# Kernel tuning notes

Hardware: AMD Instinct MI355X
Metric: run time of the kernel (lower is better)

Reference implementation:

```python
import jax, jax.numpy as jnp
import numpy as np

HIDDEN = 128
HEADS = 8
HEAD_DIM = HIDDEN // HEADS
N = 2048
SCALE = HEAD_DIM ** -0.5


def setup_inputs() -> dict:
    key = jax.random.key(0)
    ks = jax.random.split(key, 12)
    # xavier_uniform bound for square (HIDDEN, HIDDEN) weights
    bound = float(np.sqrt(6.0 / (HIDDEN + HIDDEN)))
    def w(k):
        return jax.random.uniform(k, (HIDDEN, HIDDEN), jnp.float32, -bound, bound)
    return {
        "x": jax.random.normal(ks[0], (N, HIDDEN), jnp.float32),
        "attention_bias": jax.random.normal(ks[1], (N, N, HEADS), jnp.float32),
        "key_padding_mask": jnp.zeros((N,), jnp.bool_),
        "Wq": w(ks[2]), "bq": jnp.zeros((HIDDEN,), jnp.float32),
        "Wk": w(ks[3]), "bk": jnp.zeros((HIDDEN,), jnp.float32),
        "Wv": w(ks[4]), "bv": jnp.zeros((HIDDEN,), jnp.float32),
        "Wo": w(ks[5]), "bo": jnp.zeros((HIDDEN,), jnp.float32),
    }


def reference(x, attention_bias, key_padding_mask, Wq, bq, Wk, bk, Wv, bv, Wo, bo):
    n = x.shape[0]
    # torch Linear: y = x @ W.T + b
    q = (x @ Wq.T + bq).reshape(n, HEADS, HEAD_DIM).transpose(1, 0, 2)  # (H, N, D)
    k = (x @ Wk.T + bk).reshape(n, HEADS, HEAD_DIM).transpose(1, 0, 2)
    v = (x @ Wv.T + bv).reshape(n, HEADS, HEAD_DIM).transpose(1, 0, 2)
    scores = jnp.einsum('hnd,hmd->hnm', q, k) * SCALE        # (H, N, N)
    scores = scores + attention_bias.transpose(2, 0, 1)       # additive graph bias
    mask = key_padding_mask[None, None, :]                    # (1, 1, N) over keys
    scores = jnp.where(mask, -jnp.inf, scores)
    attn = jax.nn.softmax(scores, axis=-1)
    out = jnp.einsum('hnm,hmd->hnd', attn, v)                 # (H, N, D)
    out = out.transpose(1, 0, 2).reshape(n, HIDDEN)
    return out @ Wo.T + bo
```

## Files before the change

kernel.cpp:

```cpp
#include <hip/hip_runtime.h>
#include <hip/hip_bf16.h>

#define NSEQ 2048
#define HID 128
#define HEADS 8
#define HD 16
#define SCALE 0.25f
#define TQ 8
#define TK 64
#define SPLIT 4
#define KT_PER (NSEQ / TK / SPLIT)
#define QROW 160
#define SROW 68

typedef unsigned short ushort_t;

__device__ __forceinline__ void unpack2(unsigned u, float& a, float& b) {
    union { unsigned x; float f; } lo, hi;
    lo.x = u << 16; hi.x = u & 0xffff0000u;
    a = lo.f; b = hi.f;
}
__device__ __forceinline__ void unpack8(uint4 u, float* f) {
    unpack2(u.x, f[0], f[1]); unpack2(u.y, f[2], f[3]);
    unpack2(u.z, f[4], f[5]); unpack2(u.w, f[6], f[7]);
}

__global__ void transpose_kernel(const float* __restrict__ Wq, const float* __restrict__ Wk,
                                 const float* __restrict__ Wv, const float* __restrict__ Wo,
                                 float* __restrict__ wt)
{
    int idx = blockIdx.x * 256 + threadIdx.x;
    int w = idx >> 14, rem = idx & 16383;
    int row = rem >> 7, col = rem & 127;
    const float* W = (w == 0) ? Wq : (w == 1) ? Wk : (w == 2) ? Wv : Wo;
    wt[w * 16384 + col * HID + row] = W[rem];
}

__global__ __launch_bounds__(128) void qkv_kernel(
    const float* __restrict__ x, const float* __restrict__ WqT,
    const float* __restrict__ WkT, const float* __restrict__ WvT,
    const float* __restrict__ bq, const float* __restrict__ bk,
    const float* __restrict__ bv, float* __restrict__ Qm,
    __hip_bfloat16* __restrict__ Kb, __hip_bfloat16* __restrict__ Vb)
{
    __shared__ float xs[8 * HID];
    const int j = threadIdx.x;
    const int r0 = blockIdx.x * 8;
    const float4* xg = (const float4*)(x + (size_t)r0 * HID);
    float4* xl = (float4*)xs;
    for (int i = j; i < 8 * HID / 4; i += 128) xl[i] = xg[i];
    __syncthreads();
    float aq[8], ak[8], av[8];
#pragma unroll
    for (int r = 0; r < 8; ++r) { aq[r] = 0.f; ak[r] = 0.f; av[r] = 0.f; }
    for (int i = 0; i < HID; ++i) {
        float wq = WqT[i * HID + j], wk = WkT[i * HID + j], wv = WvT[i * HID + j];
#pragma unroll
        for (int r = 0; r < 8; ++r) {
            float xv = xs[r * HID + i];
            aq[r] = fmaf(xv, wq, aq[r]);
            ak[r] = fmaf(xv, wk, ak[r]);
            av[r] = fmaf(xv, wv, av[r]);
        }
    }
    float bqv = bq[j], bkv = bk[j], bvv = bv[j];
#pragma unroll
    for (int r = 0; r < 8; ++r) {
        Qm[(size_t)(r0 + r) * HID + j] = aq[r] + bqv;
        Kb[(size_t)(r0 + r) * HID + j] = __float2bfloat16(ak[r] + bkv);
        Vb[(size_t)(r0 + r) * HID + j] = __float2bfloat16(av[r] + bvv);
    }
}

__global__ __launch_bounds__(256, 4) void attn_kernel(
    const float* __restrict__ Qm, const __hip_bfloat16* __restrict__ Kb,
    const __hip_bfloat16* __restrict__ Vb, const float* __restrict__ bias,
    const unsigned char* __restrict__ mask, float* __restrict__ Op,
    float* __restrict__ Lp)
{
    __shared__ float qs[TQ * QROW];
    __shared__ float S[TK * SROW];
    __shared__ float wl[4 * TQ * HEADS];

    const int t = threadIdx.x;
    const int qb = blockIdx.x & 255;
    const int sp = blockIdx.x >> 8;
    const int n0 = qb * TQ;

    const int sc_mp = t >> 3;
    const int sc_h  = t & 7;
    const int pv_hd = t & 127;
    const int pv_half = t >> 7;
    const int pv_h = pv_hd >> 4;
    const int pv_d = pv_hd & 15;

    {
        int r = t >> 5, c = t & 31;
        int h = c >> 2, dg = c & 3;
        float4 v = ((const float4*)(Qm + (size_t)n0 * HID))[t];
        float* dst = &qs[r * QROW + h * 20 + dg * 4];
        dst[0] = v.x; dst[1] = v.y; dst[2] = v.z; dst[3] = v.w;
    }
    float acc[TQ];
    float lsum[TQ];
#pragma unroll
    for (int r = 0; r < TQ; ++r) { acc[r] = 0.0f; lsum[r] = 0.0f; }
    __syncthreads();

    for (int kt = 0; kt < KT_PER; ++kt) {
        const int m0 = (sp * KT_PER + kt) * TK;
        {
            const int m1 = m0 + sc_mp * 2;
            float bb0[TQ], bb1[TQ];
            {
                const float* bp = bias + ((size_t)n0 * NSEQ + m1) * HEADS + sc_h;
#pragma unroll
                for (int r = 0; r < TQ; ++r) {
                    bb0[r] = __builtin_nontemporal_load(bp + (size_t)r * (NSEQ * HEADS));
                    bb1[r] = __builtin_nontemporal_load(bp + (size_t)r * (NSEQ * HEADS) + HEADS);
                }
            }
            const ushort_t* kp = (const ushort_t*)Kb + (size_t)m1 * HID + sc_h * HD;
            uint4 ka = *(const uint4*)kp;
            uint4 kb2 = *(const uint4*)(kp + 8);
            uint4 kc = *(const uint4*)(kp + HID);
            uint4 kd = *(const uint4*)(kp + HID + 8);
            float k0[16], k1[16];
            unpack8(ka, k0); unpack8(kb2, k0 + 8);
            unpack8(kc, k1); unpack8(kd, k1 + 8);
            const bool msk0 = mask[m1] != 0;
            const bool msk1 = mask[m1 + 1] != 0;
#pragma unroll
            for (int rg = 0; rg < 2; ++rg) {
                float e0[4], e1[4];
#pragma unroll
                for (int rr = 0; rr < 4; ++rr) {
                    const int r = rg * 4 + rr;
                    const float* qr = &qs[r * QROW + sc_h * 20];
                    float qf[16];
                    *(float4*)&qf[0]  = *(const float4*)(qr);
                    *(float4*)&qf[4]  = *(const float4*)(qr + 4);
                    *(float4*)&qf[8]  = *(const float4*)(qr + 8);
                    *(float4*)&qf[12] = *(const float4*)(qr + 12);
                    float d0 = 0.f, d1 = 0.f;
#pragma unroll
                    for (int i = 0; i < 16; ++i) {
                        d0 = fmaf(qf[i], k0[i], d0);
                        d1 = fmaf(qf[i], k1[i], d1);
                    }
                    float s0 = fmaf(d0, SCALE, bb0[r]);
                    float s1 = fmaf(d1, SCALE, bb1[r]);
                    if (msk0) s0 = -INFINITY;
                    if (msk1) s1 = -INFINITY;
                    float ee0 = __expf(s0);
                    float ee1 = __expf(s1);
                    lsum[r] += ee0 + ee1;
                    e0[rr] = ee0; e1[rr] = ee1;
                }
                *(float4*)&S[(2 * sc_mp) * SROW + sc_h * 8 + rg * 4] =
                    make_float4(e0[0], e0[1], e0[2], e0[3]);
                *(float4*)&S[(2 * sc_mp + 1) * SROW + sc_h * 8 + rg * 4] =
                    make_float4(e1[0], e1[1], e1[2], e1[3]);
            }
        }
        __syncthreads();
        {
            const ushort_t* vp = (const ushort_t*)Vb + (size_t)(m0 + pv_half * 32) * HID + pv_h * HD + pv_d;
#pragma unroll 4
            for (int mm = 0; mm < 32; ++mm) {
                union { unsigned x; float f; } cv;
                cv.x = ((unsigned)vp[(size_t)mm * HID]) << 16;
                const float v = cv.f;
                const float4 p0 = *(const float4*)&S[(pv_half * 32 + mm) * SROW + pv_h * 8];
                const float4 p1 = *(const float4*)&S[(pv_half * 32 + mm) * SROW + pv_h * 8 + 4];
                acc[0] = fmaf(p0.x, v, acc[0]); acc[1] = fmaf(p0.y, v, acc[1]);
                acc[2] = fmaf(p0.z, v, acc[2]); acc[3] = fmaf(p0.w, v, acc[3]);
                acc[4] = fmaf(p1.x, v, acc[4]); acc[5] = fmaf(p1.y, v, acc[5]);
                acc[6] = fmaf(p1.z, v, acc[6]); acc[7] = fmaf(p1.w, v, acc[7]);
            }
        }
        __syncthreads();
    }

#pragma unroll
    for (int r = 0; r < TQ; ++r) {
        lsum[r] += __shfl_xor(lsum[r], 8);
        lsum[r] += __shfl_xor(lsum[r], 16);
        lsum[r] += __shfl_xor(lsum[r], 32);
    }
    const int wid = t >> 6;
    if ((t & 63) < 8) {
#pragma unroll
        for (int r = 0; r < TQ; ++r)
            wl[wid * 64 + r * 8 + sc_h] = lsum[r];
    }
#pragma unroll
    for (int r = 0; r < TQ; ++r)
        S[r * 256 + pv_hd * 2 + pv_half] = acc[r];
    __syncthreads();
    if (t < 64) {
        const int r = t >> 3, h = t & 7;
        float l = wl[t] + wl[64 + t] + wl[128 + t] + wl[192 + t];
        Lp[((size_t)sp * NSEQ + n0 + r) * HEADS + h] = l;
    }
    if (t < 128) {
#pragma unroll
        for (int r = 0; r < TQ; ++r) {
            float s = S[r * 256 + t * 2] + S[r * 256 + t * 2 + 1];
            Op[((size_t)sp * NSEQ + n0 + r) * HID + t] = s;
        }
    }
}

__global__ __launch_bounds__(128) void proj_kernel(
    const float* __restrict__ Op, const float* __restrict__ Lp,
    const float* __restrict__ WoT, const float* __restrict__ bo,
    float* __restrict__ out)
{
    __shared__ float xs[8 * HID];
    const int j = threadIdx.x;
    const int r0 = blockIdx.x * 8;
    const int hh = j >> 4;
#pragma unroll
    for (int r = 0; r < 8; ++r) {
        const size_t n = r0 + r;
        float s = 0.f, l = 0.f;
#pragma unroll
        for (int sp = 0; sp < SPLIT; ++sp) {
            s += Op[((size_t)sp * NSEQ + n) * HID + j];
            l += Lp[((size_t)sp * NSEQ + n) * HEADS + hh];
        }
        xs[r * HID + j] = s / l;
    }
    __syncthreads();
    float acc[8];
#pragma unroll
    for (int r = 0; r < 8; ++r) acc[r] = 0.f;
    for (int i = 0; i < HID; ++i) {
        float w = WoT[i * HID + j];
#pragma unroll
        for (int r = 0; r < 8; ++r) acc[r] = fmaf(xs[r * HID + i], w, acc[r]);
    }
    float b = bo[j];
#pragma unroll
    for (int r = 0; r < 8; ++r)
        out[(size_t)(r0 + r) * HID + j] = acc[r] + b;
}

extern "C" void kernel_launch(void* const* d_in, const int* in_sizes, int n_in,
                              void* d_out, int out_size, void* d_ws, size_t ws_size,
                              hipStream_t stream) {
    const float* x    = (const float*)d_in[0];
    const float* bias = (const float*)d_in[1];
    const unsigned char* mask = (const unsigned char*)d_in[2];
    const float* Wq = (const float*)d_in[3];
    const float* bq = (const float*)d_in[4];
    const float* Wk = (const float*)d_in[5];
    const float* bk = (const float*)d_in[6];
    const float* Wv = (const float*)d_in[7];
    const float* bv = (const float*)d_in[8];
    const float* Wo = (const float*)d_in[9];
    const float* bo = (const float*)d_in[10];
    float* out = (float*)d_out;

    float* w = (float*)d_ws;
    float* WqT = w;
    float* WkT = w + 16384;
    float* WvT = w + 32768;
    float* WoT = w + 49152;
    float* Qm  = w + 65536;
    __hip_bfloat16* Kb = (__hip_bfloat16*)(w + 327680);
    __hip_bfloat16* Vb = (__hip_bfloat16*)(w + 458752);
    float* Op  = w + 589824;
    float* Lp  = w + 589824 + SPLIT * NSEQ * HID;

    transpose_kernel<<<256, 256, 0, stream>>>(Wq, Wk, Wv, Wo, w);
    qkv_kernel<<<NSEQ / 8, 128, 0, stream>>>(x, WqT, WkT, WvT, bq, bk, bv, Qm, Kb, Vb);
    attn_kernel<<<256 * SPLIT, 256, 0, stream>>>(Qm, Kb, Vb, bias, mask, Op, Lp);
    proj_kernel<<<NSEQ / 8, 128, 0, stream>>>(Op, Lp, WoT, bo, out);
}
```

Before: 287.0 us.

## Use bf16 MFMA for PV, transposed V, larger query tiles, split QKV launch

```diff
diff --git a/kernel.cpp b/kernel.cpp
--- a/kernel.cpp
+++ b/kernel.cpp
@@ -6,14 +6,17 @@
 #define HEADS 8
 #define HD 16
 #define SCALE 0.25f
-#define TQ 8
+#define TQ 16
 #define TK 64
-#define SPLIT 4
+#define SPLIT 8
 #define KT_PER (NSEQ / TK / SPLIT)
 #define QROW 160
-#define SROW 68
+#define PM_W 36
+#define PH_W (16 * PM_W + 4)
 
 typedef unsigned short ushort_t;
+typedef __attribute__((ext_vector_type(8))) short short8;
+typedef __attribute__((ext_vector_type(4))) float floatx4;
 
 __device__ __forceinline__ void unpack2(unsigned u, float& a, float& b) {
     union { unsigned x; float f; } lo, hi;
@@ -23,6 +26,11 @@
 __device__ __forceinline__ void unpack8(uint4 u, float* f) {
     unpack2(u.x, f[0], f[1]); unpack2(u.y, f[2], f[3]);
     unpack2(u.z, f[4], f[5]); unpack2(u.w, f[6], f[7]);
+}
+__device__ __forceinline__ unsigned pack_bf16x2(float a, float b) {
+    __hip_bfloat16 ba = __float2bfloat16(a);
+    __hip_bfloat16 bb = __float2bfloat16(b);
+    return (unsigned)*(ushort_t*)&ba | ((unsigned)*(ushort_t*)&bb << 16);
 }
 
 __global__ void transpose_kernel(const float* __restrict__ Wq, const float* __restrict__ Wk,
@@ -41,85 +49,89 @@
     const float* __restrict__ WkT, const float* __restrict__ WvT,
     const float* __restrict__ bq, const float* __restrict__ bk,
     const float* __restrict__ bv, float* __restrict__ Qm,
-    __hip_bfloat16* __restrict__ Kb, __hip_bfloat16* __restrict__ Vb)
+    __hip_bfloat16* __restrict__ Kb, __hip_bfloat16* __restrict__ Vt)
 {
     __shared__ float xs[8 * HID];
     const int j = threadIdx.x;
-    const int r0 = blockIdx.x * 8;
+    const int mat = blockIdx.x >> 8;
+    const int rb = blockIdx.x & 255;
+    const int r0 = rb * 8;
+    const float* WT = (mat == 0) ? WqT : (mat == 1) ? WkT : WvT;
+    const float* bb = (mat == 0) ? bq : (mat == 1) ? bk : bv;
     const float4* xg = (const float4*)(x + (size_t)r0 * HID);
     float4* xl = (float4*)xs;
     for (int i = j; i < 8 * HID / 4; i += 128) xl[i] = xg[i];
     __syncthreads();
-    float aq[8], ak[8], av[8];
-#pragma unroll
-    for (int r = 0; r < 8; ++r) { aq[r] = 0.f; ak[r] = 0.f; av[r] = 0.f; }
+    float acc[8];
+#pragma unroll
+    for (int r = 0; r < 8; ++r) acc[r] = 0.f;
+#pragma unroll 4
     for (int i = 0; i < HID; ++i) {
-        float wq = WqT[i * HID + j], wk = WkT[i * HID + j], wv = WvT[i * HID + j];
-#pragma unroll
-        for (int r = 0; r < 8; ++r) {
-            float xv = xs[r * HID + i];
-            aq[r] = fmaf(xv, wq, aq[r]);
-            ak[r] = fmaf(xv, wk, ak[r]);
-            av[r] = fmaf(xv, wv, av[r]);
-        }
-    }
-    float bqv = bq[j], bkv = bk[j], bvv = bv[j];
-#pragma unroll
-    for (int r = 0; r < 8; ++r) {
-        Qm[(size_t)(r0 + r) * HID + j] = aq[r] + bqv;
-        Kb[(size_t)(r0 + r) * HID + j] = __float2bfloat16(ak[r] + bkv);
-        Vb[(size_t)(r0 + r) * HID + j] = __float2bfloat16(av[r] + bvv);
+        float w = WT[i * HID + j];
+#pragma unroll
+        for (int r = 0; r < 8; ++r) acc[r] = fmaf(xs[r * HID + i], w, acc[r]);
+    }
+    float bv_ = bb[j];
+#pragma unroll
+    for (int r = 0; r < 8; ++r) acc[r] += bv_;
+    if (mat == 0) {
+#pragma unroll
+        for (int r = 0; r < 8; ++r) Qm[(size_t)(r0 + r) * HID + j] = acc[r];
+    } else if (mat == 1) {
+#pragma unroll
+        for (int r = 0; r < 8; ++r) Kb[(size_t)(r0 + r) * HID + j] = __float2bfloat16(acc[r]);
+    } else {
+        unsigned u[4];
+#pragma unroll
+        for (int p = 0; p < 4; ++p) u[p] = pack_bf16x2(acc[2 * p], acc[2 * p + 1]);
+        *(uint4*)((ushort_t*)Vt + (size_t)j * NSEQ + r0) = make_uint4(u[0], u[1], u[2], u[3]);
     }
 }
 
 __global__ __launch_bounds__(256, 4) void attn_kernel(
     const float* __restrict__ Qm, const __hip_bfloat16* __restrict__ Kb,
-    const __hip_bfloat16* __restrict__ Vb, const float* __restrict__ bias,
+    const __hip_bfloat16* __restrict__ Vt, const float* __restrict__ bias,
     const unsigned char* __restrict__ mask, float* __restrict__ Op,
     float* __restrict__ Lp)
 {
     __shared__ float qs[TQ * QROW];
-    __shared__ float S[TK * SROW];
+    __shared__ float Pbuf[8 * PH_W];
     __shared__ float wl[4 * TQ * HEADS];
 
     const int t = threadIdx.x;
-    const int qb = blockIdx.x & 255;
-    const int sp = blockIdx.x >> 8;
+    const int lane = t & 63;
+    const int wid = t >> 6;
+    const int qb = blockIdx.x & 127;
+    const int sp = blockIdx.x >> 7;
     const int n0 = qb * TQ;
 
     const int sc_mp = t >> 3;
     const int sc_h  = t & 7;
-    const int pv_hd = t & 127;
-    const int pv_half = t >> 7;
-    const int pv_h = pv_hd >> 4;
-    const int pv_d = pv_hd & 15;
+    const int kk = wid & 1;
+    const int hbase = (wid >> 1) * 4;
+    const int frag_m = lane & 15;
+    const int frag_q = lane >> 4;
 
     {
-        int r = t >> 5, c = t & 31;
-        int h = c >> 2, dg = c & 3;
-        float4 v = ((const float4*)(Qm + (size_t)n0 * HID))[t];
-        float* dst = &qs[r * QROW + h * 20 + dg * 4];
-        dst[0] = v.x; dst[1] = v.y; dst[2] = v.z; dst[3] = v.w;
-    }
-    float acc[TQ];
+        for (int idx = t; idx < 512; idx += 256) {
+            int r = idx >> 5, c = idx & 31;
+            int h = c >> 2, dg = c & 3;
+            float4 v = ((const float4*)(Qm + (size_t)n0 * HID))[idx];
+            *(float4*)&qs[r * QROW + h * 20 + dg * 4] = v;
+        }
+    }
+    floatx4 acc[4];
+#pragma unroll
+    for (int hh = 0; hh < 4; ++hh) acc[hh] = (floatx4){0.f, 0.f, 0.f, 0.f};
     float lsum[TQ];
 #pragma unroll
-    for (int r = 0; r < TQ; ++r) { acc[r] = 0.0f; lsum[r] = 0.0f; }
+    for (int r = 0; r < TQ; ++r) lsum[r] = 0.0f;
     __syncthreads();
 
     for (int kt = 0; kt < KT_PER; ++kt) {
         const int m0 = (sp * KT_PER + kt) * TK;
         {
             const int m1 = m0 + sc_mp * 2;
-            float bb0[TQ], bb1[TQ];
-            {
-                const float* bp = bias + ((size_t)n0 * NSEQ + m1) * HEADS + sc_h;
-#pragma unroll
-                for (int r = 0; r < TQ; ++r) {
-                    bb0[r] = __builtin_nontemporal_load(bp + (size_t)r * (NSEQ * HEADS));
-                    bb1[r] = __builtin_nontemporal_load(bp + (size_t)r * (NSEQ * HEADS) + HEADS);
-                }
-            }
             const ushort_t* kp = (const ushort_t*)Kb + (size_t)m1 * HID + sc_h * HD;
             uint4 ka = *(const uint4*)kp;
             uint4 kb2 = *(const uint4*)(kp + 8);
@@ -130,12 +142,19 @@
             unpack8(kc, k1); unpack8(kd, k1 + 8);
             const bool msk0 = mask[m1] != 0;
             const bool msk1 = mask[m1 + 1] != 0;
+            unsigned* Pw = (unsigned*)Pbuf;
 #pragma unroll
             for (int rg = 0; rg < 2; ++rg) {
-                float e0[4], e1[4];
-#pragma unroll
-                for (int rr = 0; rr < 4; ++rr) {
-                    const int r = rg * 4 + rr;
+                float bb0[8], bb1[8];
+                const float* bp = bias + (((size_t)(n0 + rg * 8)) * NSEQ + m1) * HEADS + sc_h;
+#pragma unroll
+                for (int rr = 0; rr < 8; ++rr) {
+                    bb0[rr] = __builtin_nontemporal_load(bp + (size_t)rr * (NSEQ * HEADS));
+                    bb1[rr] = __builtin_nontemporal_load(bp + (size_t)rr * (NSEQ * HEADS) + HEADS);
+                }
+#pragma unroll
+                for (int rr = 0; rr < 8; ++rr) {
+                    const int r = rg * 8 + rr;
                     const float* qr = &qs[r * QROW + sc_h * 20];
                     float qf[16];
                     *(float4*)&qf[0]  = *(const float4*)(qr);
@@ -148,35 +167,28 @@
                         d0 = fmaf(qf[i], k0[i], d0);
                         d1 = fmaf(qf[i], k1[i], d1);
                     }
-                    float s0 = fmaf(d0, SCALE, bb0[r]);
-                    float s1 = fmaf(d1, SCALE, bb1[r]);
+                    float s0 = fmaf(d0, SCALE, bb0[rr]);
+                    float s1 = fmaf(d1, SCALE, bb1[rr]);
                     if (msk0) s0 = -INFINITY;
                     if (msk1) s1 = -INFINITY;
-                    float ee0 = __expf(s0);
-                    float ee1 = __expf(s1);
-                    lsum[r] += ee0 + ee1;
-                    e0[rr] = ee0; e1[rr] = ee1;
+                    float e0 = __expf(s0);
+                    float e1 = __expf(s1);
+                    lsum[r] += e0 + e1;
+                    Pw[sc_h * PH_W + r * PM_W + sc_mp] = pack_bf16x2(e0, e1);
                 }
-                *(float4*)&S[(2 * sc_mp) * SROW + sc_h * 8 + rg * 4] =
-                    make_float4(e0[0], e0[1], e0[2], e0[3]);
-                *(float4*)&S[(2 * sc_mp + 1) * SROW + sc_h * 8 + rg * 4] =
-                    make_float4(e1[0], e1[1], e1[2], e1[3]);
             }
         }
         __syncthreads();
         {
-            const ushort_t* vp = (const ushort_t*)Vb + (size_t)(m0 + pv_half * 32) * HID + pv_h * HD + pv_d;
-#pragma unroll 4
-            for (int mm = 0; mm < 32; ++mm) {
-                union { unsigned x; float f; } cv;
-                cv.x = ((unsigned)vp[(size_t)mm * HID]) << 16;
-                const float v = cv.f;
-                const float4 p0 = *(const float4*)&S[(pv_half * 32 + mm) * SROW + pv_h * 8];
-                const float4 p1 = *(const float4*)&S[(pv_half * 32 + mm) * SROW + pv_h * 8 + 4];
-                acc[0] = fmaf(p0.x, v, acc[0]); acc[1] = fmaf(p0.y, v, acc[1]);
-                acc[2] = fmaf(p0.z, v, acc[2]); acc[3] = fmaf(p0.w, v, acc[3]);
-                acc[4] = fmaf(p1.x, v, acc[4]); acc[5] = fmaf(p1.y, v, acc[5]);
-                acc[6] = fmaf(p1.z, v, acc[6]); acc[7] = fmaf(p1.w, v, acc[7]);
+            const unsigned* Pw = (const unsigned*)Pbuf;
+#pragma unroll
+            for (int hh = 0; hh < 4; ++hh) {
+                const int h = hbase + hh;
+                const ushort_t* vrow = (const ushort_t*)Vt +
+                    ((size_t)(h * HD + frag_m)) * NSEQ + m0 + kk * 32 + frag_q * 8;
+                short8 bfrag = *(const short8*)vrow;
+                short8 afrag = *(const short8*)&Pw[h * PH_W + frag_m * PM_W + kk * 16 + frag_q * 4];
+                acc[hh] = __builtin_amdgcn_mfma_f32_16x16x32_bf16(afrag, bfrag, acc[hh], 0, 0, 0);
             }
         }
         __syncthreads();
@@ -188,27 +200,35 @@
         lsum[r] += __shfl_xor(lsum[r], 16);
         lsum[r] += __shfl_xor(lsum[r], 32);
     }
-    const int wid = t >> 6;
-    if ((t & 63) < 8) {
+    if (lane < 8) {
 #pragma unroll
         for (int r = 0; r < TQ; ++r)
-            wl[wid * 64 + r * 8 + sc_h] = lsum[r];
-    }
-#pragma unroll
-    for (int r = 0; r < TQ; ++r)
-        S[r * 256 + pv_hd * 2 + pv_half] = acc[r];
+            wl[wid * (TQ * HEADS) + r * 8 + lane] = lsum[r];
+    }
+    {
+        float* obuf = Pbuf;
+#pragma unroll
+        for (int hh = 0; hh < 4; ++hh) {
+#pragma unroll
+            for (int reg = 0; reg < 4; ++reg) {
+                int m = frag_q * 4 + reg;
+                obuf[kk * 2048 + (hbase + hh) * 256 + m * 16 + frag_m] = acc[hh][reg];
+            }
+        }
+    }
     __syncthreads();
-    if (t < 64) {
-        const int r = t >> 3, h = t & 7;
-        float l = wl[t] + wl[64 + t] + wl[128 + t] + wl[192 + t];
-        Lp[((size_t)sp * NSEQ + n0 + r) * HEADS + h] = l;
-    }
     if (t < 128) {
+        const float* obuf = Pbuf;
 #pragma unroll
         for (int r = 0; r < TQ; ++r) {
-            float s = S[r * 256 + t * 2] + S[r * 256 + t * 2 + 1];
-            Op[((size_t)sp * NSEQ + n0 + r) * HID + t] = s;
-        }
+            int h = t >> 4, d = t & 15;
+            float v = obuf[h * 256 + r * 16 + d] + obuf[2048 + h * 256 + r * 16 + d];
+            Op[((size_t)sp * NSEQ + n0 + r) * HID + t] = v;
+        }
+        const int r2 = t >> 3, h2 = t & 7;
+        float l = wl[r2 * 8 + h2] + wl[128 + r2 * 8 + h2] +
+                  wl[256 + r2 * 8 + h2] + wl[384 + r2 * 8 + h2];
+        Lp[((size_t)sp * NSEQ + n0 + r2) * HEADS + h2] = l;
     }
 }
 
@@ -217,12 +237,12 @@
     const float* __restrict__ WoT, const float* __restrict__ bo,
     float* __restrict__ out)
 {
-    __shared__ float xs[8 * HID];
+    __shared__ float xs[4 * HID];
     const int j = threadIdx.x;
-    const int r0 = blockIdx.x * 8;
+    const int r0 = blockIdx.x * 4;
     const int hh = j >> 4;
 #pragma unroll
-    for (int r = 0; r < 8; ++r) {
+    for (int r = 0; r < 4; ++r) {
         const size_t n = r0 + r;
         float s = 0.f, l = 0.f;
 #pragma unroll
@@ -233,17 +253,18 @@
         xs[r * HID + j] = s / l;
     }
     __syncthreads();
-    float acc[8];
-#pragma unroll
-    for (int r = 0; r < 8; ++r) acc[r] = 0.f;
+    float acc[4];
+#pragma unroll
+    for (int r = 0; r < 4; ++r) acc[r] = 0.f;
+#pragma unroll 4
     for (int i = 0; i < HID; ++i) {
         float w = WoT[i * HID + j];
 #pragma unroll
-        for (int r = 0; r < 8; ++r) acc[r] = fmaf(xs[r * HID + i], w, acc[r]);
+        for (int r = 0; r < 4; ++r) acc[r] = fmaf(xs[r * HID + i], w, acc[r]);
     }
     float b = bo[j];
 #pragma unroll
-    for (int r = 0; r < 8; ++r)
+    for (int r = 0; r < 4; ++r)
         out[(size_t)(r0 + r) * HID + j] = acc[r] + b;
 }
 
@@ -270,12 +291,12 @@
     float* WoT = w + 49152;
     float* Qm  = w + 65536;
     __hip_bfloat16* Kb = (__hip_bfloat16*)(w + 327680);
-    __hip_bfloat16* Vb = (__hip_bfloat16*)(w + 458752);
+    __hip_bfloat16* Vt = (__hip_bfloat16*)(w + 458752);
     float* Op  = w + 589824;
-    float* Lp  = w + 589824 + SPLIT * NSEQ * HID;
+    float* Lp  = w + 589824 + (size_t)SPLIT * NSEQ * HID;
 
     transpose_kernel<<<256, 256, 0, stream>>>(Wq, Wk, Wv, Wo, w);
-    qkv_kernel<<<NSEQ / 8, 128, 0, stream>>>(x, WqT, WkT, WvT, bq, bk, bv, Qm, Kb, Vb);
-    attn_kernel<<<256 * SPLIT, 256, 0, stream>>>(Qm, Kb, Vb, bias, mask, Op, Lp);
-    proj_kernel<<<NSEQ / 8, 128, 0, stream>>>(Op, Lp, WoT, bo, out);
-}
+    qkv_kernel<<<768, 128, 0, stream>>>(x, WqT, WkT, WvT, bq, bk, bv, Qm, Kb, Vt);
+    attn_kernel<<<128 * SPLIT, 256, 0, stream>>>(Qm, Kb, Vt, bias, mask, Op, Lp);
+    proj_kernel<<<512, 128, 0, stream>>>(Op, Lp, WoT, bo, out);
+}
```

After: 242.9 us. 15.3% less time.
